# Kernel tuning notes

Hardware: AMD Instinct MI355X
Metric: run time of the kernel (lower is better)

## Reference

```python
import jax, jax.numpy as jnp
import numpy as np

N_NODES = 50000


def gcn_conv(x, src, dst, W, b, n_nodes):
    """PyG GCNConv: add self-loops, symmetric D^-1/2 (A+I) D^-1/2 normalization,
    linear transform, scatter-add aggregation, bias."""
    loop = jnp.arange(n_nodes, dtype=src.dtype)
    s = jnp.concatenate([src, loop])
    d = jnp.concatenate([dst, loop])
    deg = jax.ops.segment_sum(jnp.ones_like(s, dtype=x.dtype), d, num_segments=n_nodes)
    dinv = jnp.where(deg > 0, jax.lax.rsqrt(deg), 0.0)
    norm = dinv[s] * dinv[d]                      # [E+N]
    h = x @ W                                     # [N, out] dense GEMM first (PyG order)
    msg = h[s] * norm[:, None]                    # gather + scale: [E+N, out]
    out = jax.ops.segment_sum(msg, d, num_segments=n_nodes)  # scatter-add
    return out + b


def setup_inputs() -> dict:
    key = jax.random.key(0)
    k = jax.random.split(key, 4)
    N, E, IN, HID, OUT = N_NODES, 625000, 128, 128, 64
    return {
        "x": jax.random.normal(k[0], (N, IN), jnp.float32),
        "edge_index": jax.random.randint(k[1], (2, E), 0, N, dtype=jnp.int32),
        "W1": jax.random.normal(k[2], (IN, HID), jnp.float32) / np.float32(np.sqrt(IN)),
        "b1": jnp.zeros((HID,), jnp.float32),
        "W2": jax.random.normal(k[3], (HID, OUT), jnp.float32) / np.float32(np.sqrt(HID)),
        "b2": jnp.zeros((OUT,), jnp.float32),
    }


def reference(x, edge_index, W1, b1, W2, b2):
    src, dst = edge_index[0], edge_index[1]
    # n_layers = 2: conv1 + ReLU, then final conv without activation
    h = jax.nn.relu(gcn_conv(x, src, dst, W1, b1, N_NODES))
    return gcn_conv(h, src, dst, W2, b2, N_NODES)
```

## Files before the change

### kernel.cpp

```cpp
#include <hip/hip_runtime.h>
#include <math.h>


#define RPB1 16
#define RPBO 32
#define CAP 8192
#define PA_BLK 256

typedef _Float16 h8  __attribute__((ext_vector_type(8)));
typedef _Float16 h2t __attribute__((ext_vector_type(2)));
typedef float    f4v __attribute__((ext_vector_type(4)));

__device__ __forceinline__ unsigned pkh(float a, float b) {
    auto r = __builtin_amdgcn_cvt_pkrtz(a, b);
    return __builtin_bit_cast(unsigned, r);
}
__device__ __forceinline__ void accw(float* g, float c, unsigned w) {
    h2t p = __builtin_bit_cast(h2t, w);
    g[0] += c * (float)p.x;
    g[1] += c * (float)p.y;
}
__device__ __forceinline__ void acc8h(float* ga, float c, uint4 u) {
    accw(ga + 0, c, u.x); accw(ga + 2, c, u.y);
    accw(ga + 4, c, u.z); accw(ga + 6, c, u.w);
}

__global__ __launch_bounds__(256) void k_prep(const int* __restrict__ src,
                                              const int* __restrict__ dst, int e,
                                              int* __restrict__ bcur,
                                              unsigned* __restrict__ ebuf, int EPB,
                                              const float* __restrict__ W1,
                                              const float* __restrict__ W2,
                                              unsigned short* __restrict__ Wpk1,
                                              unsigned short* __restrict__ Wpk2) {
    const int blk = (int)blockIdx.x;
    if (blk < PA_BLK) {
        __shared__ int h[256];
        __shared__ int gb[256];
        const int t = threadIdx.x;
        h[t] = 0;
        __syncthreads();
        const int e0 = blk * EPB;
        const int e1 = min(e0 + EPB, e);
        for (int i = e0 + t; i < e1; i += 256)
            atomicAdd(&h[((unsigned)dst[i]) >> 8], 1);
        __syncthreads();
        const int c = h[t];
        if (c > 0) gb[t] = atomicAdd(&bcur[t], c);
        h[t] = 0;
        __syncthreads();
        for (int i = e0 + t; i < e1; i += 256) {
            const unsigned d  = (unsigned)dst[i];
            const int bk = d >> 8;
            const int p  = atomicAdd(&h[bk], 1) + gb[bk];
            if (p < CAP) ebuf[((size_t)bk << 13) + p] = ((d & 255u) << 24) | (unsigned)src[i];
        }
    } else if (blk < PA_BLK + 8) {
        int idx = (blk - PA_BLK) * 256 + threadIdx.x;
        int l = idx & 63, g = idx >> 6;
        int kt = g >> 3, nt = g & 7;
        const float* Wp = W1 + (size_t)(kt * 32 + ((l >> 4) << 3)) * 128 + nt * 16 + (l & 15);
        uint4 o;
        o.x = pkh(Wp[0],   Wp[128]);
        o.y = pkh(Wp[256], Wp[384]);
        o.z = pkh(Wp[512], Wp[640]);
        o.w = pkh(Wp[768], Wp[896]);
        *(uint4*)&Wpk1[(size_t)idx * 8] = o;
    } else {
        int idx = (blk - PA_BLK - 8) * 256 + threadIdx.x;
        if (idx < 1024) {
            int l = idx & 63, g = idx >> 6;
            int kt = g >> 2, nt = g & 3;
            const float* Wp = W2 + (size_t)(kt * 32 + ((l >> 4) << 3)) * 64 + nt * 16 + (l & 15);
            uint4 o;
            o.x = pkh(Wp[0],   Wp[64]);
            o.y = pkh(Wp[128], Wp[192]);
            o.z = pkh(Wp[256], Wp[320]);
            o.w = pkh(Wp[384], Wp[448]);
            *(uint4*)&Wpk2[(size_t)idx * 8] = o;
        }
    }
}

__global__ __launch_bounds__(256) void k_bucket(const unsigned* __restrict__ ebuf,
                                                const int* __restrict__ bcur,
                                                int* __restrict__ rowptr,
                                                float* __restrict__ dinv,
                                                unsigned* __restrict__ erec,
                                                int n, int nbk, int e) {
    __shared__ int sc[256];
    __shared__ int h[256];
    __shared__ int loc[256];
    __shared__ int sBase;
    const int t = threadIdx.x;
    const int b = blockIdx.x;

    const int v = (t < nbk) ? min(bcur[t], CAP) : 0;
    sc[t] = v;
    __syncthreads();
    for (int off = 1; off < 256; off <<= 1) {
        int u = (t >= off) ? sc[t - off] : 0;
        __syncthreads();
        sc[t] += u;
        __syncthreads();
    }
    if (t == b) sBase = sc[t] - v;
    if (b == 0 && t == 0) rowptr[n] = e;
    h[t] = 0;
    __syncthreads();

    const int cb = min(bcur[b], CAP);
    const unsigned* __restrict__ eb = ebuf + ((size_t)b << 13);
    for (int i = t; i < cb; i += 256) atomicAdd(&h[eb[i] >> 24], 1);
    __syncthreads();
    const int deg = h[t];
    sc[t] = deg;
    __syncthreads();
    for (int off = 1; off < 256; off <<= 1) {
        int u = (t >= off) ? sc[t - off] : 0;
        __syncthreads();
        sc[t] += u;
        __syncthreads();
    }
    loc[t] = sc[t] - deg;
    const int id = (b << 8) + t;
    if (id < n) {
        rowptr[id] = sBase + loc[t];
        dinv[id]   = rsqrtf((float)(deg + 1));
    }
    h[t] = 0;
    __syncthreads();
    unsigned* __restrict__ outp = erec + sBase;
    for (int i = t; i < cb; i += 256) {
        const unsigned r  = eb[i];
        const int      lb = r >> 24;
        const int      p  = atomicAdd(&h[lb], 1);
        outp[loc[lb] + p] = r & 0xFFFFFFu;
    }
}

__global__ __launch_bounds__(256) void k_scale(const float* __restrict__ x,
                                               const float* __restrict__ dinv,
                                               unsigned short* __restrict__ xs,
                                               unsigned short* __restrict__ h2s,
                                               int n) {
    const int gid = blockIdx.x * 256 + threadIdx.x;
    const int i8  = gid * 8;
    const int row = i8 >> 7;
    if (row < n) {
        const float wd = dinv[row];
        float4 v0 = *(const float4*)&x[i8];
        float4 v1 = *(const float4*)&x[i8 + 4];
        uint4 o;
        o.x = pkh(v0.x * wd, v0.y * wd); o.y = pkh(v0.z * wd, v0.w * wd);
        o.z = pkh(v1.x * wd, v1.y * wd); o.w = pkh(v1.z * wd, v1.w * wd);
        *(uint4*)&xs[i8] = o;
    } else if (row == n) {
        *(uint4*)&xs[i8] = make_uint4(0, 0, 0, 0);
        const int k = gid - n * 16;
        if (k < 8) *(uint4*)&h2s[(size_t)n * 64 + k * 8] = make_uint4(0, 0, 0, 0);
    }
}

__global__ __launch_bounds__(256, 4) void fused_l1(const unsigned short* __restrict__ Xs,
                                                   const unsigned short* __restrict__ Wpk1,
                                                   const float* __restrict__ bias1,
                                                   const unsigned short* __restrict__ Wpk2,
                                                   const int* __restrict__ rowptr,
                                                   const unsigned* __restrict__ erec,
                                                   const float* __restrict__ dinv,
                                                   unsigned short* __restrict__ h2s,
                                                   int n) {
    __shared__ __align__(16) char sMb[RPB1 * 256];

    const int t    = threadIdx.x;
    const int row0 = blockIdx.x * RPB1;

    {
        const int r = t >> 4;
        const int b = t & 15;
        const int d = row0 + r;
        float ga[8] = {};
        if (d < n) {
            const float wd = dinv[d];
            {
                uint4 u = *((const uint4*)(Xs + ((size_t)d << 7)) + b);
                acc8h(ga, wd, u);
            }
            const int beg = rowptr[d], end = rowptr[d + 1];
            int j = beg;
            const unsigned Z = (unsigned)n;
            if (j < end) {
                unsigned s0 = (j     < end) ? erec[j]     : Z;
                unsigned s1 = (j + 1 < end) ? erec[j + 1] : Z;
                unsigned s2 = (j + 2 < end) ? erec[j + 2] : Z;
                unsigned s3 = (j + 3 < end) ? erec[j + 3] : Z;
                unsigned s4 = (j + 4 < end) ? erec[j + 4] : Z;
                unsigned s5 = (j + 5 < end) ? erec[j + 5] : Z;
                unsigned s6 = (j + 6 < end) ? erec[j + 6] : Z;
                unsigned s7 = (j + 7 < end) ? erec[j + 7] : Z;
                while (j < end) {
                    uint4 u0 = *((const uint4*)(Xs + ((size_t)s0 << 7)) + b);
                    uint4 u1 = *((const uint4*)(Xs + ((size_t)s1 << 7)) + b);
                    uint4 u2 = *((const uint4*)(Xs + ((size_t)s2 << 7)) + b);
                    uint4 u3 = *((const uint4*)(Xs + ((size_t)s3 << 7)) + b);
                    uint4 u4 = *((const uint4*)(Xs + ((size_t)s4 << 7)) + b);
                    uint4 u5 = *((const uint4*)(Xs + ((size_t)s5 << 7)) + b);
                    uint4 u6 = *((const uint4*)(Xs + ((size_t)s6 << 7)) + b);
                    uint4 u7 = *((const uint4*)(Xs + ((size_t)s7 << 7)) + b);
                    const int jn = j + 8;
                    s0 = (jn     < end) ? erec[jn]     : Z;
                    s1 = (jn + 1 < end) ? erec[jn + 1] : Z;
                    s2 = (jn + 2 < end) ? erec[jn + 2] : Z;
                    s3 = (jn + 3 < end) ? erec[jn + 3] : Z;
                    s4 = (jn + 4 < end) ? erec[jn + 4] : Z;
                    s5 = (jn + 5 < end) ? erec[jn + 5] : Z;
                    s6 = (jn + 6 < end) ? erec[jn + 6] : Z;
                    s7 = (jn + 7 < end) ? erec[jn + 7] : Z;
                    acc8h(ga, wd, u0);
                    acc8h(ga, wd, u1);
                    acc8h(ga, wd, u2);
                    acc8h(ga, wd, u3);
                    acc8h(ga, wd, u4);
                    acc8h(ga, wd, u5);
                    acc8h(ga, wd, u6);
                    acc8h(ga, wd, u7);
                    j = jn;
                }
            }
        }
        uint4 o;
        o.x = pkh(ga[0], ga[1]); o.y = pkh(ga[2], ga[3]);
        o.z = pkh(ga[4], ga[5]); o.w = pkh(ga[6], ga[7]);
        const int swz = (r & 7) << 4;
        *(uint4*)(sMb + ((r * 256 + b * 16) ^ swz)) = o;
    }
    __syncthreads();

    const int w  = t >> 6;
    const int l  = t & 63;
    const int lr = l & 15;
    const int lk = (l >> 4) << 4;
    const int sz = (lr & 7) << 4;

    f4v acc[2] = {};
#pragma unroll
    for (int kt = 0; kt < 4; ++kt) {
        const int kb = kt * 64 + lk;
        h8 a0 = *(const h8*)(sMb + ((lr * 256 + kb) ^ sz));
        const h8* Bp = (const h8*)Wpk1 + (kt * 8 + w * 2) * 64 + l;
        h8 b0 = Bp[0];
        h8 b1 = Bp[64];
        acc[0] = __builtin_amdgcn_mfma_f32_16x16x32_f16(a0, b0, acc[0], 0, 0, 0);
        acc[1] = __builtin_amdgcn_mfma_f32_16x16x32_f16(a0, b1, acc[1], 0, 0, 0);
    }
    __syncthreads();

    {
        const float bb0 = bias1[w * 32 + lr];
        const float bb1 = bias1[w * 32 + 16 + lr];
        const int c0 = (w * 32 + lr) * 2;
        const int c1 = (w * 32 + 16 + lr) * 2;
#pragma unroll
        for (int v = 0; v < 4; ++v) {
            const int row = ((l >> 4) << 2) + v;
            const int rs  = (row & 7) << 4;
            float o0 = fmaxf(acc[0][v] + bb0, 0.f);
            float o1 = fmaxf(acc[1][v] + bb1, 0.f);
            *(_Float16*)(sMb + ((row * 256 + c0) ^ rs)) = (_Float16)o0;
            *(_Float16*)(sMb + ((row * 256 + c1) ^ rs)) = (_Float16)o1;
        }
    }
    __syncthreads();

    f4v acc2 = {};
#pragma unroll
    for (int kt = 0; kt < 4; ++kt) {
        const int kb = kt * 64 + lk;
        h8 a0 = *(const h8*)(sMb + ((lr * 256 + kb) ^ sz));
        h8 b  = *((const h8*)Wpk2 + (kt * 4 + w) * 64 + l);
        acc2 = __builtin_amdgcn_mfma_f32_16x16x32_f16(a0, b, acc2, 0, 0, 0);
    }
#pragma unroll
    for (int v = 0; v < 4; ++v) {
        const int row = row0 + ((l >> 4) << 2) + v;
        if (row < n) {
            _Float16 hv = (_Float16)(acc2[v] * dinv[row]);
            h2s[(size_t)row * 64 + w * 16 + lr] = __builtin_bit_cast(unsigned short, hv);
        }
    }
}

__global__ __launch_bounds__(256, 4) void k_out(const unsigned short* __restrict__ h2s,
                                                const float* __restrict__ b2,
                                                const int* __restrict__ rowptr,
                                                const unsigned* __restrict__ erec,
                                                const float* __restrict__ dinv,
                                                float* __restrict__ out, int n) {
    const int t = threadIdx.x;
    const int r = t >> 3;
    const int b = t & 7;
    const int d = blockIdx.x * RPBO + r;
    if (d >= n) return;

    const float wd = dinv[d];
    float ga[8] = {};
    {
        uint4 u = *((const uint4*)(h2s + ((size_t)d << 6)) + b);
        acc8h(ga, wd, u);
    }
    const int beg = rowptr[d], end = rowptr[d + 1];
    int j = beg;
    const unsigned Z = (unsigned)n;
    if (j < end) {
        unsigned s0 = (j     < end) ? erec[j]     : Z;
        unsigned s1 = (j + 1 < end) ? erec[j + 1] : Z;
        unsigned s2 = (j + 2 < end) ? erec[j + 2] : Z;
        unsigned s3 = (j + 3 < end) ? erec[j + 3] : Z;
        unsigned s4 = (j + 4 < end) ? erec[j + 4] : Z;
        unsigned s5 = (j + 5 < end) ? erec[j + 5] : Z;
        unsigned s6 = (j + 6 < end) ? erec[j + 6] : Z;
        unsigned s7 = (j + 7 < end) ? erec[j + 7] : Z;
        while (j < end) {
            uint4 u0 = *((const uint4*)(h2s + ((size_t)s0 << 6)) + b);
            uint4 u1 = *((const uint4*)(h2s + ((size_t)s1 << 6)) + b);
            uint4 u2 = *((const uint4*)(h2s + ((size_t)s2 << 6)) + b);
            uint4 u3 = *((const uint4*)(h2s + ((size_t)s3 << 6)) + b);
            uint4 u4 = *((const uint4*)(h2s + ((size_t)s4 << 6)) + b);
            uint4 u5 = *((const uint4*)(h2s + ((size_t)s5 << 6)) + b);
            uint4 u6 = *((const uint4*)(h2s + ((size_t)s6 << 6)) + b);
            uint4 u7 = *((const uint4*)(h2s + ((size_t)s7 << 6)) + b);
            const int jn = j + 8;
            s0 = (jn     < end) ? erec[jn]     : Z;
            s1 = (jn + 1 < end) ? erec[jn + 1] : Z;
            s2 = (jn + 2 < end) ? erec[jn + 2] : Z;
            s3 = (jn + 3 < end) ? erec[jn + 3] : Z;
            s4 = (jn + 4 < end) ? erec[jn + 4] : Z;
            s5 = (jn + 5 < end) ? erec[jn + 5] : Z;
            s6 = (jn + 6 < end) ? erec[jn + 6] : Z;
            s7 = (jn + 7 < end) ? erec[jn + 7] : Z;
            acc8h(ga, wd, u0);
            acc8h(ga, wd, u1);
            acc8h(ga, wd, u2);
            acc8h(ga, wd, u3);
            acc8h(ga, wd, u4);
            acc8h(ga, wd, u5);
            acc8h(ga, wd, u6);
            acc8h(ga, wd, u7);
            j = jn;
        }
    }
    const float4 bv0 = *(const float4*)&b2[b * 8];
    const float4 bv1 = *(const float4*)&b2[b * 8 + 4];
    float* O = out + (size_t)d * 64 + b * 8;
    *(float4*)O       = make_float4(ga[0] + bv0.x, ga[1] + bv0.y, ga[2] + bv0.z, ga[3] + bv0.w);
    *(float4*)(O + 4) = make_float4(ga[4] + bv1.x, ga[5] + bv1.y, ga[6] + bv1.z, ga[7] + bv1.w);
}


extern "C" void kernel_launch(void* const* d_in, const int* in_sizes, int n_in,
                              void* d_out, int out_size, void* d_ws, size_t ws_size,
                              hipStream_t stream) {
    const float* x  = (const float*)d_in[0];
    const int*   ei = (const int*)d_in[1];
    const float* W1 = (const float*)d_in[2];
    const float* b1 = (const float*)d_in[3];
    const float* W2 = (const float*)d_in[4];
    const float* b2 = (const float*)d_in[5];
    float* out = (float*)d_out;

    const int N = in_sizes[0] / 128;
    const int E = in_sizes[1] / 2;
    const int* src = ei;
    const int* dst = ei + E;
    const int NBK = (N + 255) >> 8;
    if (NBK > 256) return;

    size_t off = 0;
    char* base = (char*)d_ws;
    auto carve = [&](size_t bytes) -> void* {
        void* p = base + off;
        off += (bytes + 255) & ~(size_t)255;
        return p;
    };
    int*      bcur   = (int*)carve(256 * 4);
    int*      rowptr = (int*)carve((size_t)(N + 1) * 4);
    float*    dinv   = (float*)carve((size_t)N * 4);
    unsigned* erec   = (unsigned*)carve((size_t)E * 4);
    unsigned* ebuf   = (unsigned*)carve((size_t)256 * CAP * 4);
    unsigned short* xs   = (unsigned short*)carve((size_t)(N + 1) * 128 * 2);
    unsigned short* h2s  = (unsigned short*)carve((size_t)(N + 1) * 64 * 2);
    unsigned short* Wpk1 = (unsigned short*)carve(128 * 128 * 2);
    unsigned short* Wpk2 = (unsigned short*)carve(128 * 64 * 2);

    if (off > ws_size) return;

    const int EPB = (E + PA_BLK - 1) / PA_BLK;
    hipMemsetAsync(bcur, 0, 256 * 4, stream);
    k_prep<<<PA_BLK + 12, 256, 0, stream>>>(src, dst, E, bcur, ebuf, EPB,
                                            W1, W2, Wpk1, Wpk2);
    k_bucket<<<NBK, 256, 0, stream>>>(ebuf, bcur, rowptr, dinv, erec, N, NBK, E);
    k_scale<<<((N + 1) * 16 + 255) / 256, 256, 0, stream>>>(x, dinv, xs, h2s, N);

    fused_l1<<<(N + RPB1 - 1) / RPB1, 256, 0, stream>>>(xs, Wpk1, b1, Wpk2,
                                                        rowptr, erec, dinv, h2s, N);
    k_out<<<(N + RPBO - 1) / RPBO, 256, 0, stream>>>(h2s, b2, rowptr, erec, dinv, out, N);
}
```

Baseline: 150.4 us.

## Sort rows by degree within each 256-node bucket to balance gather work

The bucket kernel now counting-sorts the nodes of each 256-node bucket by in-degree and writes a permutation. The fused layer-1 and output aggregation kernels process rows in that order, so threads in a wave handle nodes of similar degree and diverge less in their edge loops. The cost is an extra shared-memory scan in the bucket kernel, an indirection through perm, scattered output row writes, and a few extra padded blocks.

```diff
diff --git a/kernel.cpp b/kernel.cpp
--- a/kernel.cpp
+++ b/kernel.cpp
@@ -87,6 +87,7 @@
                                                 int* __restrict__ rowptr,
                                                 float* __restrict__ dinv,
                                                 unsigned* __restrict__ erec,
+                                                int* __restrict__ perm,
                                                 int n, int nbk, int e) {
     __shared__ int sc[256];
     __shared__ int h[256];
@@ -137,6 +138,23 @@
         const int      p  = atomicAdd(&h[lb], 1);
         outp[loc[lb] + p] = r & 0xFFFFFFu;
     }
+
+    __syncthreads();
+    h[t] = 0;
+    __syncthreads();
+    const int dbin = min(deg, 255);
+    const int arrival = atomicAdd(&h[dbin], 1);
+    __syncthreads();
+    sc[t] = h[t];
+    __syncthreads();
+    for (int off = 1; off < 256; off <<= 1) {
+        int u = (t >= off) ? sc[t - off] : 0;
+        __syncthreads();
+        sc[t] += u;
+        __syncthreads();
+    }
+    const int rank = sc[dbin] - h[dbin] + arrival;
+    perm[(b << 8) + rank] = (id < n) ? id : n;
 }
 
 __global__ __launch_bounds__(256) void k_scale(const float* __restrict__ x,
@@ -169,9 +187,12 @@
                                                    const int* __restrict__ rowptr,
                                                    const unsigned* __restrict__ erec,
                                                    const float* __restrict__ dinv,
+                                                   const int* __restrict__ perm,
                                                    unsigned short* __restrict__ h2s,
                                                    int n) {
     __shared__ __align__(16) char sMb[RPB1 * 256];
+    __shared__ int   sPerm[RPB1];
+    __shared__ float sDinv[RPB1];
 
     const int t    = threadIdx.x;
     const int row0 = blockIdx.x * RPB1;
@@ -179,10 +200,11 @@
     {
         const int r = t >> 4;
         const int b = t & 15;
-        const int d = row0 + r;
+        const int d = perm[row0 + r];
+        const float wd = (d < n) ? dinv[d] : 0.f;
+        if (b == 0) { sPerm[r] = d; sDinv[r] = wd; }
         float ga[8] = {};
         if (d < n) {
-            const float wd = dinv[d];
             {
                 uint4 u = *((const uint4*)(Xs + ((size_t)d << 7)) + b);
                 acc8h(ga, wd, u);
@@ -283,10 +305,11 @@
     }
 #pragma unroll
     for (int v = 0; v < 4; ++v) {
-        const int row = row0 + ((l >> 4) << 2) + v;
-        if (row < n) {
-            _Float16 hv = (_Float16)(acc2[v] * dinv[row]);
-            h2s[(size_t)row * 64 + w * 16 + lr] = __builtin_bit_cast(unsigned short, hv);
+        const int slot = ((l >> 4) << 2) + v;
+        const int node = sPerm[slot];
+        if (node < n) {
+            _Float16 hv = (_Float16)(acc2[v] * sDinv[slot]);
+            h2s[(size_t)node * 64 + w * 16 + lr] = __builtin_bit_cast(unsigned short, hv);
         }
     }
 }
@@ -296,11 +319,12 @@
                                                 const int* __restrict__ rowptr,
                                                 const unsigned* __restrict__ erec,
                                                 const float* __restrict__ dinv,
+                                                const int* __restrict__ perm,
                                                 float* __restrict__ out, int n) {
     const int t = threadIdx.x;
     const int r = t >> 3;
     const int b = t & 7;
-    const int d = blockIdx.x * RPBO + r;
+    const int d = perm[blockIdx.x * RPBO + r];
     if (d >= n) return;
 
     const float wd = dinv[d];
@@ -386,6 +410,7 @@
     int*      bcur   = (int*)carve(256 * 4);
     int*      rowptr = (int*)carve((size_t)(N + 1) * 4);
     float*    dinv   = (float*)carve((size_t)N * 4);
+    int*      perm   = (int*)carve((size_t)NBK * 256 * 4);
     unsigned* erec   = (unsigned*)carve((size_t)E * 4);
     unsigned* ebuf   = (unsigned*)carve((size_t)256 * CAP * 4);
     unsigned short* xs   = (unsigned short*)carve((size_t)(N + 1) * 128 * 2);
@@ -399,10 +424,11 @@
     hipMemsetAsync(bcur, 0, 256 * 4, stream);
     k_prep<<<PA_BLK + 12, 256, 0, stream>>>(src, dst, E, bcur, ebuf, EPB,
                                             W1, W2, Wpk1, Wpk2);
-    k_bucket<<<NBK, 256, 0, stream>>>(ebuf, bcur, rowptr, dinv, erec, N, NBK, E);
+    k_bucket<<<NBK, 256, 0, stream>>>(ebuf, bcur, rowptr, dinv, erec, perm, N, NBK, E);
     k_scale<<<((N + 1) * 16 + 255) / 256, 256, 0, stream>>>(x, dinv, xs, h2s, N);
 
-    fused_l1<<<(N + RPB1 - 1) / RPB1, 256, 0, stream>>>(xs, Wpk1, b1, Wpk2,
-                                                        rowptr, erec, dinv, h2s, N);
-    k_out<<<(N + RPBO - 1) / RPBO, 256, 0, stream>>>(h2s, b2, rowptr, erec, dinv, out, N);
-}
+    fused_l1<<<NBK * (256 / RPB1), 256, 0, stream>>>(xs, Wpk1, b1, Wpk2,
+                                                     rowptr, erec, dinv, perm, h2s, N);
+    k_out<<<NBK * (256 / RPBO), 256, 0, stream>>>(h2s, b2, rowptr, erec, dinv,
+                                                  perm, out, N);
+}
```

After: 157.2 us. 1.05x slower.
